# Kernel tuning notes

Hardware: AMD Instinct MI355X
Metric: run time of the kernel (lower is better)

## Reference

```python
import jax, jax.numpy as jnp
import numpy as np

K = 9          # temporal window (kernel_size)
PAD = (K - 1) // 2
BN_EPS = 1e-5


def setup_inputs() -> dict:
    key = jax.random.key(0)
    ks = jax.random.split(key, 9)
    N, Cin, Cout, T, V = 16, 64, 128, 256, 25
    return {
        "x": jax.random.normal(ks[0], (N, Cin, T, V), jnp.float32),
        "conv_w": jax.random.normal(ks[1], (Cout, Cin), jnp.float32) * (1.0 / np.sqrt(Cin)),
        "conv_b": jax.random.normal(ks[2], (Cout,), jnp.float32) * 0.01,
        "gamma": jax.random.uniform(ks[3], (Cout,), jnp.float32, 0.5, 1.5),
        "beta": jax.random.normal(ks[4], (Cout,), jnp.float32) * 0.1,
        "run_mean": jax.random.normal(ks[5], (Cout,), jnp.float32) * 0.1,
        "run_var": jax.random.uniform(ks[6], (Cout,), jnp.float32, 0.5, 1.5),
        "att0": jnp.full((1, Cout, 1, K), 1.0 / K, jnp.float32),
        "A": jax.random.uniform(ks[7], (V, V), jnp.float32),
        "keep_prob": 1,
    }


def reference(x, conv_w, conv_b, gamma, beta, run_mean, run_var, att0, A, keep_prob):
    # 1x1 conv (pointwise channel mix); AvgPool2d((1,1)) is identity for stride=1
    x = jnp.einsum("nctv,oc->notv", x, conv_w) + conv_b[None, :, None, None]
    # BatchNorm2d (eval mode: running stats)
    scale = gamma / jnp.sqrt(run_var + BN_EPS)
    x = x * scale[None, :, None, None] + (beta - run_mean * scale)[None, :, None, None]
    N, C, T, V = x.shape
    # UnfoldTemporalWindows: zero-pad T, gather K temporal shifts -> (N, C, T, K, V)
    xp = jnp.pad(x, ((0, 0), (0, 0), (PAD, PAD), (0, 0)))
    upfold = jnp.stack([xp[:, :, u:u + T, :] for u in range(K)], axis=3)
    # local attention: score each window position against the center frame
    scores = jnp.einsum("nctv,nctuv->nctu", x, upfold) / V
    attn = jax.nn.softmax(scores, axis=-1) + att0
    out = jnp.einsum("nctuv,nctu->nctv", upfold, attn)
    # dropS / dropT are identity at keep_prob == 1 (inference)
    return out
```

## Files before the change

### kernel.cpp

```cpp
#include <hip/hip_runtime.h>
#include <hip/hip_bf16.h>

#define CIN   64
#define COUT  128
#define TT    256
#define VV    25
#define TV    (TT * VV)
#define KW    9
#define PAD   4

#define YT_BASE 16896
#define YTSTR   280
#define S_BASE  30896
#define CF_BASE 40112
#define SMEM_SZ 44208

typedef __attribute__((ext_vector_type(8))) short short8;
typedef __attribute__((ext_vector_type(4))) float f32x4;

__device__ __forceinline__ unsigned f2b(float f) {
    unsigned u = __builtin_bit_cast(unsigned, f);
    return (u + 0x7FFFu + ((u >> 16) & 1u)) >> 16;
}
__device__ __forceinline__ float lof(unsigned u) {
    return __builtin_bit_cast(float, u << 16);
}
__device__ __forceinline__ float hif(unsigned u) {
    return __builtin_bit_cast(float, u & 0xffff0000u);
}
__device__ __forceinline__ int swz(int row, int cbyte) {
    return row * 128 + ((cbyte & ~15) ^ ((row & 7) << 4)) + (cbyte & 15);
}

__global__ __launch_bounds__(256) void conv_mfma(
    const float* __restrict__ x, const float* __restrict__ w,
    const float* __restrict__ cb, const float* __restrict__ gamma,
    const float* __restrict__ beta, const float* __restrict__ rm,
    const float* __restrict__ rv, unsigned short* __restrict__ y)
{
    __shared__ __align__(16) unsigned short Wl[COUT * 64];
    __shared__ __align__(16) unsigned short Xl[128 * 64];
    __shared__ float sc[COUT];
    __shared__ float of[COUT];

    const int pc  = blockIdx.x;
    const int n   = blockIdx.y;
    const int tid = threadIdx.x;
    const int posbase = pc * 128;

    if (tid < COUT) {
        const float s = gamma[tid] * rsqrtf(rv[tid] + 1e-5f);
        sc[tid] = s;
        of[tid] = cb[tid] * s + beta[tid] - rm[tid] * s;
    }
    for (int idx = tid; idx < 2048; idx += 256) {
        const int c4 = idx & 15, o = idx >> 4;
        const f32x4 wv = *(const f32x4*)(w + o * 64 + c4 * 4);
        uint2 pk;
        pk.x = f2b(wv.x) | (f2b(wv.y) << 16);
        pk.y = f2b(wv.z) | (f2b(wv.w) << 16);
        *(uint2*)((char*)Wl + swz(o, c4 * 8)) = pk;
    }
    for (int idx = tid; idx < 2048; idx += 256) {
        const int pos = idx & 127, c4 = idx >> 7;
        const float* xp = x + (size_t)n * CIN * TV + (size_t)(c4 * 4) * TV + posbase + pos;
        const float a0 = xp[0], a1 = xp[TV], a2 = xp[2 * TV], a3 = xp[3 * TV];
        uint2 pk;
        pk.x = f2b(a0) | (f2b(a1) << 16);
        pk.y = f2b(a2) | (f2b(a3) << 16);
        *(uint2*)((char*)Xl + swz(pos, c4 * 8)) = pk;
    }
    __syncthreads();

    const int wv_ = tid >> 6, lane = tid & 63;
    const int lr = lane & 15, lh = lane >> 4;

    short8 bw[2][2];
#pragma unroll
    for (int nn = 0; nn < 2; ++nn)
#pragma unroll
        for (int kh = 0; kh < 2; ++kh)
            bw[nn][kh] = *(const short8*)((const char*)Wl +
                              swz(wv_ * 32 + nn * 16 + lr, kh * 64 + lh * 16));

    f32x4 acc[8][2];
#pragma unroll
    for (int m = 0; m < 8; ++m)
#pragma unroll
        for (int nn = 0; nn < 2; ++nn) acc[m][nn] = (f32x4){0.f, 0.f, 0.f, 0.f};

#pragma unroll
    for (int m = 0; m < 8; ++m) {
        const int prow = m * 16 + lr;
        const short8 a0 = *(const short8*)((const char*)Xl + swz(prow, lh * 16));
        const short8 a1 = *(const short8*)((const char*)Xl + swz(prow, 64 + lh * 16));
#pragma unroll
        for (int nn = 0; nn < 2; ++nn) {
            acc[m][nn] = __builtin_amdgcn_mfma_f32_16x16x32_bf16(a0, bw[nn][0], acc[m][nn], 0, 0, 0);
            acc[m][nn] = __builtin_amdgcn_mfma_f32_16x16x32_bf16(a1, bw[nn][1], acc[m][nn], 0, 0, 0);
        }
    }

#pragma unroll
    for (int nn = 0; nn < 2; ++nn) {
        const int o = wv_ * 32 + nn * 16 + lr;
        const float s = sc[o], f = of[o];
        unsigned short* yb = y + (size_t)(n * COUT + o) * TV + posbase + lh * 4;
#pragma unroll
        for (int m = 0; m < 8; ++m) {
            const f32x4 a = acc[m][nn];
            uint2 pk;
            pk.x = f2b(a[0] * s + f) | (f2b(a[1] * s + f) << 16);
            pk.y = f2b(a[2] * s + f) | (f2b(a[3] * s + f) << 16);
            *(uint2*)(yb + m * 16) = pk;
        }
    }
}

__global__ __launch_bounds__(256) void attn_kernel(
    const unsigned short* __restrict__ y, const float* __restrict__ att0,
    float* __restrict__ out)
{
    __shared__ __align__(16) char smem[SMEM_SZ];
    __shared__ float a0s[KW];

    unsigned* yw = (unsigned*)smem;
    unsigned short* ytr = (unsigned short*)(smem + YT_BASE);

    const int nc  = blockIdx.x;
    const int c   = nc & (COUT - 1);
    const int tid = threadIdx.x;
    const int lane = tid & 63, w = tid >> 6;

    if (tid < KW) a0s[tid] = att0[c * KW + tid];

    if (tid < 8) {
        const int r = (tid < 4) ? tid : 256 + tid;
#pragma unroll
        for (int d = 0; d < 16; ++d) yw[r * 16 + d] = 0;
    }
    if (tid < 200) {
        const int v = tid >> 3, k = tid & 7;
        ((unsigned*)ytr)[v * 140 + (k < 2 ? k : 128 + k)] = 0;
    }

    {
        const unsigned* ygu = (const unsigned*)(y + (size_t)nc * TV);
        const int t = tid;
        const int s0 = (25 * t) >> 1;
        const int odd = t & 1;
        unsigned u[14];
#pragma unroll
        for (int i = 0; i < 14; ++i) u[i] = ygu[min(s0 + i, 3199)];
        unsigned rd[13];
#pragma unroll
        for (int d = 0; d < 13; ++d) {
            const unsigned sh = (u[d] >> 16) | (u[d + 1] << 16);
            rd[d] = odd ? sh : u[d];
        }
        rd[12] &= 0xffffu;
        const int r = t + 4;
        const int rx = (r & 3) ^ ((r >> 2) & 3);
#pragma unroll
        for (int d = 0; d < 13; ++d)
            yw[r * 16 + ((((d >> 2) ^ rx) << 2) | (d & 3))] = rd[d];
#pragma unroll
        for (int d = 13; d < 16; ++d)
            yw[r * 16 + (((3 ^ rx) << 2) | (d & 3))] = 0;
#pragma unroll
        for (int v = 0; v < 25; ++v) {
            const unsigned dd = rd[v >> 1];
            ytr[v * YTSTR + r] = (unsigned short)((v & 1) ? (dd >> 16) : (dd & 0xffffu));
        }
    }
    {
        uint4* cfz = (uint4*)(smem + CF_BASE + w * 1024);
        cfz[lane] = make_uint4(0, 0, 0, 0);
    }
    __syncthreads();

    float* sS = (float*)(smem + S_BASE + w * 2304);
    char* cfb = smem + CF_BASE + w * 1024;
    const int lr16 = lane & 15, q = lane >> 4;

    f32x4 ok[4][2];

#pragma unroll
    for (int ch = 0; ch < 4; ++ch) {
        const int t0 = (w * 4 + ch) * 16;

        short8 af, b1, b2;
        {
            const int ra = t0 + 4 + lr16;
            af = *(const short8*)(smem + ra * 64 + ((q ^ (ra & 3) ^ ((ra >> 2) & 3)) << 4));
            const int rb1 = t0 + lr16;
            b1 = *(const short8*)(smem + rb1 * 64 + ((q ^ (rb1 & 3) ^ ((rb1 >> 2) & 3)) << 4));
            const int rb2 = t0 + 16 + lr16;
            b2 = *(const short8*)(smem + rb2 * 64 + ((q ^ (rb2 & 3) ^ ((rb2 >> 2) & 3)) << 4));
        }
        f32x4 s1 = (f32x4){0.f, 0.f, 0.f, 0.f}, s2 = (f32x4){0.f, 0.f, 0.f, 0.f};
        s1 = __builtin_amdgcn_mfma_f32_16x16x32_bf16(af, b1, s1, 0, 0, 0);
        s2 = __builtin_amdgcn_mfma_f32_16x16x32_bf16(af, b2, s2, 0, 0, 0);

#pragma unroll
        for (int r = 0; r < 4; ++r) {
            sS[(q * 4 + r) * 36 + lr16]      = s1[r];
            sS[(q * 4 + r) * 36 + 16 + lr16] = s2[r];
        }

        if (lane < 16) {
            const int m = lane;
            float e[9], den = 0.f;
#pragma unroll
            for (int j = 0; j < 9; ++j) {
                e[j] = __expf(sS[m * 36 + m + j] * (1.f / 25.f));
                den += e[j];
            }
            const float inv = 1.f / den;
            const int mx = (m & 3) ^ ((m >> 2) & 3);
#pragma unroll
            for (int j = 0; j < 9; ++j) {
                const int n = m + j;
                const float cf = fmaf(e[j], inv, a0s[j]);
                *(unsigned short*)(cfb + m * 64 + ((((n >> 3) ^ mx) << 4) | ((n & 7) << 1)))
                    = (unsigned short)f2b(cf);
            }
        }

        short8 ac, bv1, bv2;
        {
            const int mx = (lr16 & 3) ^ ((lr16 >> 2) & 3);
            ac  = *(const short8*)(cfb + lr16 * 64 + ((q ^ mx) << 4));
            bv1 = *(const short8*)((char*)ytr + lr16 * 560 + (t0 + q * 8) * 2);
            bv2 = *(const short8*)((char*)ytr + (16 + lr16) * 560 + (t0 + q * 8) * 2);
        }
        f32x4 o1 = (f32x4){0.f, 0.f, 0.f, 0.f}, o2 = (f32x4){0.f, 0.f, 0.f, 0.f};
        o1 = __builtin_amdgcn_mfma_f32_16x16x32_bf16(ac, bv1, o1, 0, 0, 0);
        o2 = __builtin_amdgcn_mfma_f32_16x16x32_bf16(ac, bv2, o2, 0, 0, 0);
        ok[ch][0] = o1;
        ok[ch][1] = o2;
    }
    __syncthreads();

    float* ov = (float*)smem;
#pragma unroll
    for (int ch = 0; ch < 4; ++ch) {
        const int rowb = (w * 4 + ch) * 16 + q * 4;
#pragma unroll
        for (int r = 0; r < 4; ++r) {
            ov[(rowb + r) * 25 + lr16] = ok[ch][0][r];
            if (lr16 < 9)
                ov[(rowb + r) * 25 + 16 + lr16] = ok[ch][1][r];
        }
    }
    __syncthreads();
    {
        float4* og = (float4*)(out + (size_t)nc * TV);
        const float4* sm4 = (const float4*)smem;
#pragma unroll
        for (int i = 0; i < 7; ++i) {
            const int ci = tid + i * 256;
            if (ci < TV / 4) og[ci] = sm4[ci];
        }
    }
}

extern "C" void kernel_launch(void* const* d_in, const int* in_sizes, int n_in,
                              void* d_out, int out_size, void* d_ws, size_t ws_size,
                              hipStream_t stream)
{
    const float* x     = (const float*)d_in[0];
    const float* w     = (const float*)d_in[1];
    const float* cb    = (const float*)d_in[2];
    const float* gamma = (const float*)d_in[3];
    const float* beta  = (const float*)d_in[4];
    const float* rm    = (const float*)d_in[5];
    const float* rv    = (const float*)d_in[6];
    const float* att0  = (const float*)d_in[7];
    float* out = (float*)d_out;
    unsigned short* y = (unsigned short*)d_ws;

    dim3 gA(TV / 128, 16);
    conv_mfma<<<gA, 256, 0, stream>>>(x, w, cb, gamma, beta, rm, rv, y);

    dim3 gB(16 * COUT);
    attn_kernel<<<gB, 256, 0, stream>>>(y, att0, out);
}
```

Before: 44.64 us.

## Process four channels per attention block with register-prefetched next tile

The attention kernel now loops over four (n,c) slices per block, with a grid of 512 blocks instead of 2048. While the current slice is computed, the next slice's y data and att0 weights are loaded into registers (double-buffered). The output staging area is separated from the input tiles so loads can overlap compute. The aim is to hide global-load latency and amortise block launch cost. In exchange, shared memory grows to about 70KB per block and register pressure rises, which lowers occupancy and leaves fewer blocks to fill the CUs.

```diff
diff --git a/kernel.cpp b/kernel.cpp
--- a/kernel.cpp
+++ b/kernel.cpp
@@ -9,11 +9,12 @@
 #define KW    9
 #define PAD   4
 
-#define YT_BASE 16896
-#define YTSTR   280
-#define S_BASE  30896
-#define CF_BASE 40112
-#define SMEM_SZ 44208
+#define OV_B    0
+#define YTILE_B 25600
+#define YTR_B   42496
+#define S_B     56496
+#define CF_B    65712
+#define SMEM_SZ 69808
 
 typedef __attribute__((ext_vector_type(8))) short short8;
 typedef __attribute__((ext_vector_type(4))) float f32x4;
@@ -122,17 +123,16 @@
     float* __restrict__ out)
 {
     __shared__ __align__(16) char smem[SMEM_SZ];
-    __shared__ float a0s[KW];
-
-    unsigned* yw = (unsigned*)smem;
-    unsigned short* ytr = (unsigned short*)(smem + YT_BASE);
-
-    const int nc  = blockIdx.x;
-    const int c   = nc & (COUT - 1);
+
+    const int bid = blockIdx.x;
     const int tid = threadIdx.x;
     const int lane = tid & 63, w = tid >> 6;
-
-    if (tid < KW) a0s[tid] = att0[c * KW + tid];
+    const int lr16 = lane & 15, q = lane >> 4;
+
+    unsigned* yw = (unsigned*)(smem + YTILE_B);
+    unsigned short* ytr = (unsigned short*)(smem + YTR_B);
+    float* sS = (float*)(smem + S_B + w * 2304);
+    char* cfb = smem + CF_B + w * 1024;
 
     if (tid < 8) {
         const int r = (tid < 4) ? tid : 256 + tid;
@@ -143,124 +143,147 @@
         const int v = tid >> 3, k = tid & 7;
         ((unsigned*)ytr)[v * 140 + (k < 2 ? k : 128 + k)] = 0;
     }
-
     {
-        const unsigned* ygu = (const unsigned*)(y + (size_t)nc * TV);
-        const int t = tid;
-        const int s0 = (25 * t) >> 1;
-        const int odd = t & 1;
-        unsigned u[14];
-#pragma unroll
-        for (int i = 0; i < 14; ++i) u[i] = ygu[min(s0 + i, 3199)];
-        unsigned rd[13];
-#pragma unroll
-        for (int d = 0; d < 13; ++d) {
-            const unsigned sh = (u[d] >> 16) | (u[d + 1] << 16);
-            rd[d] = odd ? sh : u[d];
-        }
-        rd[12] &= 0xffffu;
-        const int r = t + 4;
-        const int rx = (r & 3) ^ ((r >> 2) & 3);
-#pragma unroll
-        for (int d = 0; d < 13; ++d)
-            yw[r * 16 + ((((d >> 2) ^ rx) << 2) | (d & 3))] = rd[d];
-#pragma unroll
-        for (int d = 13; d < 16; ++d)
-            yw[r * 16 + (((3 ^ rx) << 2) | (d & 3))] = 0;
-#pragma unroll
-        for (int v = 0; v < 25; ++v) {
-            const unsigned dd = rd[v >> 1];
-            ytr[v * YTSTR + r] = (unsigned short)((v & 1) ? (dd >> 16) : (dd & 0xffffu));
-        }
-    }
+        uint4* cfz = (uint4*)(smem + CF_B + w * 1024);
+        cfz[lane] = make_uint4(0, 0, 0, 0);
+    }
+
+    const int s0 = (25 * tid) >> 1;
+    const int odd = tid & 1;
+
+    unsigned u[2][14];
+    float a0v[2][9];
+
     {
-        uint4* cfz = (uint4*)(smem + CF_BASE + w * 1024);
-        cfz[lane] = make_uint4(0, 0, 0, 0);
-    }
-    __syncthreads();
-
-    float* sS = (float*)(smem + S_BASE + w * 2304);
-    char* cfb = smem + CF_BASE + w * 1024;
-    const int lr16 = lane & 15, q = lane >> 4;
-
-    f32x4 ok[4][2];
-
-#pragma unroll
-    for (int ch = 0; ch < 4; ++ch) {
-        const int t0 = (w * 4 + ch) * 16;
-
-        short8 af, b1, b2;
+        const unsigned* yg = (const unsigned*)(y + (size_t)(bid * 4) * TV);
+#pragma unroll
+        for (int i = 0; i < 14; ++i) u[0][i] = yg[min(s0 + i, 3199)];
+        const int c0 = (bid * 4) & (COUT - 1);
+#pragma unroll
+        for (int j = 0; j < 9; ++j) a0v[0][j] = att0[c0 * KW + j];
+    }
+
+#pragma unroll
+    for (int p = 0; p < 4; ++p) {
+        const int cur = p & 1, nxt = cur ^ 1;
+        const size_t nc = (size_t)(bid * 4 + p);
+
         {
-            const int ra = t0 + 4 + lr16;
-            af = *(const short8*)(smem + ra * 64 + ((q ^ (ra & 3) ^ ((ra >> 2) & 3)) << 4));
-            const int rb1 = t0 + lr16;
-            b1 = *(const short8*)(smem + rb1 * 64 + ((q ^ (rb1 & 3) ^ ((rb1 >> 2) & 3)) << 4));
-            const int rb2 = t0 + 16 + lr16;
-            b2 = *(const short8*)(smem + rb2 * 64 + ((q ^ (rb2 & 3) ^ ((rb2 >> 2) & 3)) << 4));
-        }
-        f32x4 s1 = (f32x4){0.f, 0.f, 0.f, 0.f}, s2 = (f32x4){0.f, 0.f, 0.f, 0.f};
-        s1 = __builtin_amdgcn_mfma_f32_16x16x32_bf16(af, b1, s1, 0, 0, 0);
-        s2 = __builtin_amdgcn_mfma_f32_16x16x32_bf16(af, b2, s2, 0, 0, 0);
-
-#pragma unroll
-        for (int r = 0; r < 4; ++r) {
-            sS[(q * 4 + r) * 36 + lr16]      = s1[r];
-            sS[(q * 4 + r) * 36 + 16 + lr16] = s2[r];
-        }
-
-        if (lane < 16) {
-            const int m = lane;
-            float e[9], den = 0.f;
-#pragma unroll
-            for (int j = 0; j < 9; ++j) {
-                e[j] = __expf(sS[m * 36 + m + j] * (1.f / 25.f));
-                den += e[j];
-            }
-            const float inv = 1.f / den;
-            const int mx = (m & 3) ^ ((m >> 2) & 3);
-#pragma unroll
-            for (int j = 0; j < 9; ++j) {
-                const int n = m + j;
-                const float cf = fmaf(e[j], inv, a0s[j]);
-                *(unsigned short*)(cfb + m * 64 + ((((n >> 3) ^ mx) << 4) | ((n & 7) << 1)))
-                    = (unsigned short)f2b(cf);
-            }
-        }
-
-        short8 ac, bv1, bv2;
+            unsigned rd[13];
+#pragma unroll
+            for (int d = 0; d < 13; ++d) {
+                const unsigned sh = (u[cur][d] >> 16) | (u[cur][d + 1] << 16);
+                rd[d] = odd ? sh : u[cur][d];
+            }
+            rd[12] &= 0xffffu;
+            const int r = tid + 4;
+            const int rx = (r & 3) ^ ((r >> 2) & 3);
+#pragma unroll
+            for (int d = 0; d < 13; ++d)
+                yw[r * 16 + ((((d >> 2) ^ rx) << 2) | (d & 3))] = rd[d];
+#pragma unroll
+            for (int d = 13; d < 16; ++d)
+                yw[r * 16 + (((3 ^ rx) << 2) | (d & 3))] = 0;
+#pragma unroll
+            for (int v = 0; v < 25; ++v) {
+                const unsigned dd = rd[v >> 1];
+                ytr[v * 280 + r] = (unsigned short)((v & 1) ? (dd >> 16) : (dd & 0xffffu));
+            }
+        }
+        __syncthreads();
+
+        if (p < 3) {
+            const unsigned* yg = (const unsigned*)(y + (nc + 1) * TV);
+#pragma unroll
+            for (int i = 0; i < 14; ++i) u[nxt][i] = yg[min(s0 + i, 3199)];
+            const int cn = (int)((nc + 1) & (COUT - 1));
+#pragma unroll
+            for (int j = 0; j < 9; ++j) a0v[nxt][j] = att0[cn * KW + j];
+        }
+
+        f32x4 ok[4][2];
+#pragma unroll
+        for (int ch = 0; ch < 4; ++ch) {
+            const int t0 = (w * 4 + ch) * 16;
+
+            short8 af, b1, b2;
+            {
+                const int ra = t0 + 4 + lr16;
+                af = *(const short8*)(smem + YTILE_B + ra * 64 +
+                                      ((q ^ (ra & 3) ^ ((ra >> 2) & 3)) << 4));
+                const int rb1 = t0 + lr16;
+                b1 = *(const short8*)(smem + YTILE_B + rb1 * 64 +
+                                      ((q ^ (rb1 & 3) ^ ((rb1 >> 2) & 3)) << 4));
+                const int rb2 = t0 + 16 + lr16;
+                b2 = *(const short8*)(smem + YTILE_B + rb2 * 64 +
+                                      ((q ^ (rb2 & 3) ^ ((rb2 >> 2) & 3)) << 4));
+            }
+            f32x4 s1 = (f32x4){0.f, 0.f, 0.f, 0.f}, s2 = (f32x4){0.f, 0.f, 0.f, 0.f};
+            s1 = __builtin_amdgcn_mfma_f32_16x16x32_bf16(af, b1, s1, 0, 0, 0);
+            s2 = __builtin_amdgcn_mfma_f32_16x16x32_bf16(af, b2, s2, 0, 0, 0);
+
+#pragma unroll
+            for (int r = 0; r < 4; ++r) {
+                sS[(q * 4 + r) * 36 + lr16]      = s1[r];
+                sS[(q * 4 + r) * 36 + 16 + lr16] = s2[r];
+            }
+
+            if (lane < 16) {
+                const int m = lane;
+                float e[9], den = 0.f;
+#pragma unroll
+                for (int j = 0; j < 9; ++j) {
+                    e[j] = __expf(sS[m * 36 + m + j] * (1.f / 25.f));
+                    den += e[j];
+                }
+                const float inv = 1.f / den;
+                const int mx = (m & 3) ^ ((m >> 2) & 3);
+#pragma unroll
+                for (int j = 0; j < 9; ++j) {
+                    const int n = m + j;
+                    const float cf = fmaf(e[j], inv, a0v[cur][j]);
+                    *(unsigned short*)(cfb + m * 64 + ((((n >> 3) ^ mx) << 4) | ((n & 7) << 1)))
+                        = (unsigned short)f2b(cf);
+                }
+            }
+
+            short8 ac, bv1, bv2;
+            {
+                const int mx = (lr16 & 3) ^ ((lr16 >> 2) & 3);
+                ac  = *(const short8*)(cfb + lr16 * 64 + ((q ^ mx) << 4));
+                bv1 = *(const short8*)((char*)ytr + lr16 * 560 + (t0 + q * 8) * 2);
+                bv2 = *(const short8*)((char*)ytr + (16 + lr16) * 560 + (t0 + q * 8) * 2);
+            }
+            f32x4 o1 = (f32x4){0.f, 0.f, 0.f, 0.f}, o2 = (f32x4){0.f, 0.f, 0.f, 0.f};
+            o1 = __builtin_amdgcn_mfma_f32_16x16x32_bf16(ac, bv1, o1, 0, 0, 0);
+            o2 = __builtin_amdgcn_mfma_f32_16x16x32_bf16(ac, bv2, o2, 0, 0, 0);
+            ok[ch][0] = o1;
+            ok[ch][1] = o2;
+        }
+        __syncthreads();
+
         {
-            const int mx = (lr16 & 3) ^ ((lr16 >> 2) & 3);
-            ac  = *(const short8*)(cfb + lr16 * 64 + ((q ^ mx) << 4));
-            bv1 = *(const short8*)((char*)ytr + lr16 * 560 + (t0 + q * 8) * 2);
-            bv2 = *(const short8*)((char*)ytr + (16 + lr16) * 560 + (t0 + q * 8) * 2);
-        }
-        f32x4 o1 = (f32x4){0.f, 0.f, 0.f, 0.f}, o2 = (f32x4){0.f, 0.f, 0.f, 0.f};
-        o1 = __builtin_amdgcn_mfma_f32_16x16x32_bf16(ac, bv1, o1, 0, 0, 0);
-        o2 = __builtin_amdgcn_mfma_f32_16x16x32_bf16(ac, bv2, o2, 0, 0, 0);
-        ok[ch][0] = o1;
-        ok[ch][1] = o2;
-    }
-    __syncthreads();
-
-    float* ov = (float*)smem;
-#pragma unroll
-    for (int ch = 0; ch < 4; ++ch) {
-        const int rowb = (w * 4 + ch) * 16 + q * 4;
-#pragma unroll
-        for (int r = 0; r < 4; ++r) {
-            ov[(rowb + r) * 25 + lr16] = ok[ch][0][r];
-            if (lr16 < 9)
-                ov[(rowb + r) * 25 + 16 + lr16] = ok[ch][1][r];
-        }
-    }
-    __syncthreads();
-    {
-        float4* og = (float4*)(out + (size_t)nc * TV);
-        const float4* sm4 = (const float4*)smem;
-#pragma unroll
-        for (int i = 0; i < 7; ++i) {
-            const int ci = tid + i * 256;
-            if (ci < TV / 4) og[ci] = sm4[ci];
+            float* ov = (float*)smem;
+#pragma unroll
+            for (int ch = 0; ch < 4; ++ch) {
+                const int rowb = (w * 4 + ch) * 16 + q * 4;
+#pragma unroll
+                for (int r = 0; r < 4; ++r) {
+                    ov[(rowb + r) * 25 + lr16] = ok[ch][0][r];
+                    if (lr16 < 9)
+                        ov[(rowb + r) * 25 + 16 + lr16] = ok[ch][1][r];
+                }
+            }
+        }
+        __syncthreads();
+        {
+            float4* og = (float4*)(out + nc * TV);
+            const float4* sm4 = (const float4*)smem;
+#pragma unroll
+            for (int i = 0; i < 7; ++i) {
+                const int ci = tid + i * 256;
+                if (ci < TV / 4) og[ci] = sm4[ci];
+            }
         }
     }
 }
@@ -283,6 +306,6 @@
     dim3 gA(TV / 128, 16);
     conv_mfma<<<gA, 256, 0, stream>>>(x, w, cb, gamma, beta, rm, rv, y);
 
-    dim3 gB(16 * COUT);
+    dim3 gB(512);
     attn_kernel<<<gB, 256, 0, stream>>>(y, att0, out);
 }
```

Result: slower. 46.63 us (+4.4%).
